# Optimization experiments

Measured on AMD Instinct MI355X. Metric: run time of the kernel, lower is better.

The kernel has to match this reference:

```python
import jax, jax.numpy as jnp
import numpy as np

B, M, D = 16384, 40, 32
INPUT_DIM = M * D  # 1280
CIN_SIZES = [128, 128]
DEEP_DIMS = [256, 128, 64]
EPS = 1e-5


def _init_linear(key, fan_in, fan_out):
    k1, k2 = jax.random.split(key)
    bound = 1.0 / np.sqrt(fan_in)
    w = jax.random.uniform(k1, (fan_out, fan_in), jnp.float32, -bound, bound)
    b = jax.random.uniform(k2, (fan_out,), jnp.float32, -bound, bound)
    return w, b


def setup_inputs() -> dict:
    key = jax.random.key(0)
    ks = jax.random.split(key, 12)
    x = jax.random.normal(ks[0], (B, INPUT_DIM), jnp.float32)
    emb_3d = jax.random.normal(ks[1], (B, M, D), jnp.float32)
    lin_w, lin_b = _init_linear(ks[2], INPUT_DIM, 1)
    # CIN conv1d (kernel_size=1) weights, flattened to [out, in]
    conv_w0, conv_b0 = _init_linear(ks[3], M * M, CIN_SIZES[0])          # in = 40*40
    prev1 = CIN_SIZES[0] // 2                                             # split_half
    conv_w1, conv_b1 = _init_linear(ks[4], M * prev1, CIN_SIZES[1])       # in = 40*64
    cin_out_dim = CIN_SIZES[0] // 2 + CIN_SIZES[1]                        # 192
    cin_out_w, cin_out_b = _init_linear(ks[5], cin_out_dim, 1)
    dims = [INPUT_DIM] + DEEP_DIMS
    deep_w0, deep_b0 = _init_linear(ks[6], dims[0], dims[1])
    deep_w1, deep_b1 = _init_linear(ks[7], dims[1], dims[2])
    deep_w2, deep_b2 = _init_linear(ks[8], dims[2], dims[3])
    ln_g0, ln_b0 = jnp.ones((dims[1],), jnp.float32), jnp.zeros((dims[1],), jnp.float32)
    ln_g1, ln_b1 = jnp.ones((dims[2],), jnp.float32), jnp.zeros((dims[2],), jnp.float32)
    ln_g2, ln_b2 = jnp.ones((dims[3],), jnp.float32), jnp.zeros((dims[3],), jnp.float32)
    return dict(x=x, emb_3d=emb_3d, lin_w=lin_w, lin_b=lin_b,
                conv_w0=conv_w0, conv_b0=conv_b0, conv_w1=conv_w1, conv_b1=conv_b1,
                cin_out_w=cin_out_w, cin_out_b=cin_out_b,
                deep_w0=deep_w0, deep_b0=deep_b0, ln_g0=ln_g0, ln_b0=ln_b0,
                deep_w1=deep_w1, deep_b1=deep_b1, ln_g1=ln_g1, ln_b1=ln_b1,
                deep_w2=deep_w2, deep_b2=deep_b2, ln_g2=ln_g2, ln_b2=ln_b2)


def _layernorm(h, g, b):
    mu = jnp.mean(h, axis=-1, keepdims=True)
    var = jnp.mean(jnp.square(h - mu), axis=-1, keepdims=True)
    return (h - mu) * jax.lax.rsqrt(var + EPS) * g + b


def _cin_layer(x0, xi, w, b):
    # outer = einsum('bmd,bnd->bmnd') then 1x1 conv over flattened (m*n).
    # Fused: contract the (m,n) outer product directly with the conv weight.
    o = w.shape[0]
    m, n = x0.shape[1], xi.shape[1]
    w3 = w.reshape(o, m, n)
    out = jnp.einsum('bmd,bnd,omn->bod', x0, xi, w3) + b[None, :, None]
    return jax.nn.relu(out)


def reference(x, emb_3d, lin_w, lin_b,
              conv_w0, conv_b0, conv_w1, conv_b1, cin_out_w, cin_out_b,
              deep_w0, deep_b0, ln_g0, ln_b0,
              deep_w1, deep_b1, ln_g1, ln_b1,
              deep_w2, deep_b2, ln_g2, ln_b2):
    aux = (x @ lin_w.T + lin_b)[:, 0]  # [B]

    # CIN with split_half=True
    x0 = emb_3d                                   # [B, 40, 32]
    out0 = _cin_layer(x0, x0, conv_w0, conv_b0)    # [B, 128, 32]
    h1, direct0 = jnp.split(out0, 2, axis=1)       # hidden gets FIRST half
    out1 = _cin_layer(x0, h1, conv_w1, conv_b1)    # [B, 128, 32]
    cin_feat = jnp.sum(jnp.concatenate([direct0, out1], axis=1), axis=2)  # [B, 192]
    aux = aux + (cin_feat @ cin_out_w.T + cin_out_b)[:, 0]

    # Deep tower (dropout = identity in eval)
    h = jax.nn.relu(_layernorm(x @ deep_w0.T + deep_b0, ln_g0, ln_b0))
    h = jax.nn.relu(_layernorm(h @ deep_w1.T + deep_b1, ln_g1, ln_b1))
    h = jax.nn.relu(_layernorm(h @ deep_w2.T + deep_b2, ln_g2, ln_b2))
    return h, aux
```

## Files before the change

kernel.cpp:

```cpp
#include <hip/hip_runtime.h>
#include <hip/hip_bf16.h>

typedef unsigned int u32;
typedef __attribute__((ext_vector_type(8))) short short8;
typedef __attribute__((ext_vector_type(8))) _Float16 half8;
typedef __attribute__((ext_vector_type(4))) float f32x4;

__device__ __forceinline__ u32 bf16_rne(float f) {
  u32 u = __builtin_bit_cast(u32, f);
  return (u + 0x7fffu + ((u >> 16) & 1u)) >> 16;
}
__device__ __forceinline__ u32 pk_bf16(float a, float b) {
  union { __hip_bfloat162 h; u32 u; } cv;
  cv.h = __float22bfloat162_rn(make_float2(a, b));
  return cv.u;
}
__device__ __forceinline__ unsigned short f16b(float f) {
  return __builtin_bit_cast(unsigned short, (_Float16)f);
}
__device__ __forceinline__ half8 splat8(_Float16 x) {
  return (half8){x, x, x, x, x, x, x, x};
}

__device__ __forceinline__ void glds16(const u32* g, u32* l) {
  __builtin_amdgcn_global_load_lds((const __attribute__((address_space(1))) u32*)g,
                                   (__attribute__((address_space(3))) u32*)l, 16, 0, 0);
}

__global__ void swz_kernel(const float* __restrict__ W, unsigned short* __restrict__ out,
                           int N, int K) {
  int tid = blockIdx.x * 256 + threadIdx.x;
  if (tid >= N * K) return;
  int j = tid & 7, l = (tid >> 3) & 63, rest = tid >> 9;
  int nt = N >> 4;
  int t = rest % nt, k32 = rest / nt;
  int o = t * 16 + (l & 15);
  int k = k32 * 32 + (l >> 4) * 8 + j;
  out[tid] = (unsigned short)bf16_rne(W[(size_t)o * K + k]);
}
__global__ void swz_f16_kernel(const float* __restrict__ W, unsigned short* __restrict__ out,
                               int N, int K) {
  int tid = blockIdx.x * 256 + threadIdx.x;
  if (tid >= N * K) return;
  int j = tid & 7, l = (tid >> 3) & 63, rest = tid >> 9;
  int nt = N >> 4;
  int t = rest % nt, k32 = rest / nt;
  int o = t * 16 + (l & 15);
  int k = k32 * 32 + (l >> 4) * 8 + j;
  out[tid] = f16b(W[(size_t)o * K + k]);
}

__global__ void tbl_kernel(u32* __restrict__ tbl0) {
  int g = threadIdx.x;
  if (g >= 120) return;
  int base = 0, m = 0;
  for (m = 0; m < 40; ++m) {
    int cnt = 5 - (m >> 3);
    if (g < base + cnt) break;
    base += cnt;
  }
  int n0 = 8 * ((m >> 3) + (g - base));
  tbl0[g] = (u32)m | ((u32)n0 << 8);
}

__global__ void swz0s_kernel(const float* __restrict__ W, const u32* __restrict__ tbl0,
                             unsigned short* __restrict__ out) {
  int tid = blockIdx.x * 256 + threadIdx.x;
  if (tid >= 960 * 128) return;
  int j = tid & 7, l = (tid >> 3) & 63, rest = tid >> 9;
  int t = rest & 7, k32 = rest >> 3;
  int o = t * 16 + (l & 15);
  int g = k32 * 4 + (l >> 4);
  u32 te = tbl0[g];
  int m = (int)(te & 255u), n0 = (int)(te >> 8);
  int n = n0 + j;
  float val;
  if (n < m) val = 0.f;
  else if (n == m) val = W[o * 1600 + m * 41];
  else val = W[o * 1600 + m * 40 + n] + W[o * 1600 + n * 40 + m];
  out[tid] = f16b(val);
}

__global__ void lin_kernel(const float* __restrict__ x, const float* __restrict__ lw,
                           const float* __restrict__ lb, const float* __restrict__ cb,
                           float* __restrict__ aux) {
  int row = blockIdx.x * 4 + (threadIdx.x >> 6);
  int lane = threadIdx.x & 63;
  const float* xr = x + (size_t)row * 1280;
  float s = 0.f;
#pragma unroll
  for (int e = 0; e < 20; ++e) s += xr[e * 64 + lane] * lw[e * 64 + lane];
#pragma unroll
  for (int m = 1; m < 64; m <<= 1) s += __shfl_xor(s, m, 64);
  if (lane == 0) aux[row] = s + lb[0] + cb[0];
}

__global__ __launch_bounds__(256, 4) void cin_kernel(
    const float* __restrict__ emb, const unsigned short* __restrict__ wz0s,
    const unsigned short* __restrict__ wz1, const u32* __restrict__ tbl0,
    const float* __restrict__ b0v, const float* __restrict__ b1v,
    const float* __restrict__ cw, float* __restrict__ aux) {
  __shared__ unsigned short Xh[128 * 44];
  __shared__ unsigned short h1s[128 * 68];
  __shared__ u32 tbl[120];
  __shared__ float auxacc[128];

  const int tid = threadIdx.x;
  const int lane = tid & 63;
  const int w = tid >> 6;
  const int wr = w >> 1, wc = w & 1;
  const int rl = lane & 15, q = lane >> 4;
  const int b0blk = blockIdx.x * 4;

#pragma unroll
  for (int i = 0; i < 5; ++i) {
    int idx = i * 256 + tid;
    int b = idx / 320;
    int rem = idx - b * 320;
    int m = rem >> 3, d0 = (rem & 7) * 4;
    float4 v = *(const float4*)(emb + ((size_t)(b0blk + b) * 40 + m) * 32 + d0);
    unsigned short* xc = &Xh[(b * 32 + d0) * 44 + m];
    xc[0] = f16b(v.x); xc[44] = f16b(v.y); xc[88] = f16b(v.z); xc[132] = f16b(v.w);
  }
  if (tid < 128) auxacc[tid] = 0.f;
  if (tid < 120) tbl[tid] = tbl0[tid];
  __syncthreads();

  f32x4 acc[4][4];
#pragma unroll
  for (int u = 0; u < 4; ++u)
#pragma unroll
    for (int t = 0; t < 4; ++t) acc[u][t] = f32x4{0.f, 0.f, 0.f, 0.f};

  {
    const u32* bptr = (const u32*)wz0s + wc * 1024 + lane * 4;
    uint4 bA[4], bB[4];
#pragma unroll
    for (int tt = 0; tt < 4; ++tt) bA[tt] = *(const uint4*)(bptr + tt * 256);

    auto chunk0 = [&](int kc, uint4* bv) {
      u32 te = tbl[kc * 4 + q];
      int mm = (int)(te & 255u);
      int w0 = (int)(te >> 8) >> 1;
#pragma unroll
      for (int u = 0; u < 4; ++u) {
        int r = 64 * wr + 16 * u + rl;
        const u32* xr = (const u32*)&Xh[r * 44];
        uint4 vn = *(const uint4*)&xr[w0];
        _Float16 xm = __builtin_bit_cast(_Float16, Xh[r * 44 + mm]);
        half8 af = __builtin_bit_cast(half8, vn) * splat8(xm);
#pragma unroll
        for (int tt = 0; tt < 4; ++tt)
          acc[u][tt] = __builtin_amdgcn_mfma_f32_16x16x32_f16(
              af, __builtin_bit_cast(half8, bv[tt]), acc[u][tt], 0, 0, 0);
      }
    };

    for (int kc = 0; kc < 30; kc += 2) {
#pragma unroll
      for (int tt = 0; tt < 4; ++tt)
        bB[tt] = *(const uint4*)(bptr + (kc + 1) * 2048 + tt * 256);
      chunk0(kc, bA);
      int kn2 = (kc + 2 < 30) ? kc + 2 : 0;
#pragma unroll
      for (int tt = 0; tt < 4; ++tt)
        bA[tt] = *(const uint4*)(bptr + kn2 * 2048 + tt * 256);
      chunk0(kc + 1, bB);
    }
  }

  if (wc == 0) {
#pragma unroll
    for (int u = 0; u < 4; ++u) {
      int r0q = 64 * wr + 16 * u + 4 * q;
#pragma unroll
      for (int tt = 0; tt < 4; ++tt) {
        int o = 16 * tt + rl;
        float bb = b0v[o];
#pragma unroll
        for (int i = 0; i < 4; ++i) {
          float vv = fmaxf(acc[u][tt][i] + bb, 0.f);
          h1s[(r0q + i) * 68 + o] = f16b(vv);
        }
      }
    }
  } else {
#pragma unroll
    for (int u = 0; u < 4; ++u)
#pragma unroll
      for (int i = 0; i < 4; ++i) {
        float sle = 0.f;
#pragma unroll
        for (int tt = 0; tt < 4; ++tt) {
          int o = 64 + 16 * tt + rl;
          sle += fmaxf(acc[u][tt][i] + b0v[o], 0.f) * cw[o - 64];
        }
        sle += __shfl_xor(sle, 1, 16);
        sle += __shfl_xor(sle, 2, 16);
        sle += __shfl_xor(sle, 4, 16);
        sle += __shfl_xor(sle, 8, 16);
        if (rl == 0) atomicAdd(&auxacc[64 * wr + 16 * u + 4 * q + i], sle);
      }
  }
#pragma unroll
  for (int u = 0; u < 4; ++u)
#pragma unroll
    for (int t = 0; t < 4; ++t) acc[u][t] = f32x4{0.f, 0.f, 0.f, 0.f};
  __syncthreads();

  {
    const u32* bptr = (const u32*)wz1 + wc * 1024 + lane * 4;
    uint4 bA[4], bB[4];
#pragma unroll
    for (int tt = 0; tt < 4; ++tt) bA[tt] = *(const uint4*)(bptr + tt * 256);

    auto chunk1 = [&](int kc, uint4* bv) {
      int mm = kc >> 1;
      int wof = ((kc & 1) << 4) + 4 * q;
#pragma unroll
      for (int u = 0; u < 4; ++u) {
        int r = 64 * wr + 16 * u + rl;
        uint4 hp = *(const uint4*)((const u32*)h1s + r * 34 + wof);
        _Float16 xm = __builtin_bit_cast(_Float16, Xh[r * 44 + mm]);
        half8 af = __builtin_bit_cast(half8, hp) * splat8(xm);
#pragma unroll
        for (int tt = 0; tt < 4; ++tt)
          acc[u][tt] = __builtin_amdgcn_mfma_f32_16x16x32_f16(
              af, __builtin_bit_cast(half8, bv[tt]), acc[u][tt], 0, 0, 0);
      }
    };

    for (int kc = 0; kc < 80; kc += 2) {
#pragma unroll
      for (int tt = 0; tt < 4; ++tt)
        bB[tt] = *(const uint4*)(bptr + (kc + 1) * 2048 + tt * 256);
      chunk1(kc, bA);
      int kn2 = (kc + 2 < 80) ? kc + 2 : 0;
#pragma unroll
      for (int tt = 0; tt < 4; ++tt)
        bA[tt] = *(const uint4*)(bptr + kn2 * 2048 + tt * 256);
      chunk1(kc + 1, bB);
    }
  }

#pragma unroll
  for (int u = 0; u < 4; ++u)
#pragma unroll
    for (int i = 0; i < 4; ++i) {
      float sle = 0.f;
#pragma unroll
      for (int tt = 0; tt < 4; ++tt) {
        int o = 64 * wc + 16 * tt + rl;
        sle += fmaxf(acc[u][tt][i] + b1v[o], 0.f) * cw[64 + o];
      }
      sle += __shfl_xor(sle, 1, 16);
      sle += __shfl_xor(sle, 2, 16);
      sle += __shfl_xor(sle, 4, 16);
      sle += __shfl_xor(sle, 8, 16);
      if (rl == 0) atomicAdd(&auxacc[64 * wr + 16 * u + 4 * q + i], sle);
    }
  __syncthreads();
  if (tid < 4) {
    float ssum = 0.f;
    for (int d = 0; d < 32; ++d) ssum += auxacc[tid * 32 + d];
    aux[b0blk + tid] += ssum;
  }
}

template <int NT, bool AF32>
__global__ __launch_bounds__(256, 2) void gemm_deep(
    const void* __restrict__ Ain, const unsigned short* __restrict__ Bswz,
    const float* __restrict__ bias, float* __restrict__ Cout, int M, int N, int K) {
  __shared__ unsigned short At[128 * 40];
  __shared__ u32 Bt[NT * 256];
  const int tid = threadIdx.x, lane = tid & 63, w = tid >> 6;
  const int wr = w >> 1, wc = w & 1, rl = lane & 15, q = lane >> 4;
  const int r0 = blockIdx.x * 128, c0 = blockIdx.y * (NT * 16);
  const int ntg = N >> 4;
  constexpr int WT = NT / 2;
  f32x4 acc[4][WT];
#pragma unroll
  for (int u = 0; u < 4; ++u)
#pragma unroll
    for (int t = 0; t < WT; ++t) acc[u][t] = f32x4{0.f, 0.f, 0.f, 0.f};

  for (int kk = 0; kk < K; kk += 32) {
    __syncthreads();
    {
      int r = tid >> 1, kh = (tid & 1) * 16;
      if constexpr (AF32) {
        const float* A = (const float*)Ain;
        const float* src = A + (size_t)(r0 + r) * K + kk + kh;
        float4 v0 = *(const float4*)src;
        float4 v1 = *(const float4*)(src + 4);
        float4 v2 = *(const float4*)(src + 8);
        float4 v3 = *(const float4*)(src + 12);
        uint4 p0, p1;
        p0.x = pk_bf16(v0.x, v0.y); p0.y = pk_bf16(v0.z, v0.w);
        p0.z = pk_bf16(v1.x, v1.y); p0.w = pk_bf16(v1.z, v1.w);
        p1.x = pk_bf16(v2.x, v2.y); p1.y = pk_bf16(v2.z, v2.w);
        p1.z = pk_bf16(v3.x, v3.y); p1.w = pk_bf16(v3.z, v3.w);
        uint4* dst = (uint4*)&At[r * 40 + kh];
        dst[0] = p0;
        dst[1] = p1;
      } else {
        const unsigned short* A = (const unsigned short*)Ain;
        const uint4* src = (const uint4*)(A + (size_t)(r0 + r) * K + kk + kh);
        uint4* dst = (uint4*)&At[r * 40 + kh];
        dst[0] = src[0];
        dst[1] = src[1];
      }
      const u32* gb = (const u32*)Bswz + ((size_t)(kk >> 5) * ntg + (c0 >> 4)) * 256;
      constexpr int WW = NT * 64;
#pragma unroll
      for (int j = 0; j < NT / 4; ++j)
        glds16(gb + w * WW + j * 256 + lane * 4, &Bt[w * WW + j * 256]);
    }
    __syncthreads();
    short8 af[4];
#pragma unroll
    for (int u = 0; u < 4; ++u) {
      int rt = 4 * wr + u;
      uint4 av = *(const uint4*)&At[(16 * rt + rl) * 40 + q * 8];
      af[u] = __builtin_bit_cast(short8, av);
    }
#pragma unroll
    for (int tt = 0; tt < WT; ++tt) {
      int tg = WT * wc + tt;
      uint4 bv = *(const uint4*)&Bt[(tg * 64 + lane) * 4];
      short8 bfv = __builtin_bit_cast(short8, bv);
#pragma unroll
      for (int u = 0; u < 4; ++u)
        acc[u][tt] = __builtin_amdgcn_mfma_f32_16x16x32_bf16(af[u], bfv, acc[u][tt], 0, 0, 0);
    }
  }
#pragma unroll
  for (int u = 0; u < 4; ++u) {
    int rr = r0 + 64 * wr + 16 * u + 4 * q;
#pragma unroll
    for (int tt = 0; tt < WT; ++tt) {
      int o = c0 + (WT * wc + tt) * 16 + rl;
      float bb = bias[o];
#pragma unroll
      for (int i = 0; i < 4; ++i)
        Cout[(size_t)(rr + i) * N + o] = acc[u][tt][i] + bb;
    }
  }
}

template <int D, bool OUTF32>
__global__ void ln_relu_kernel(const float* __restrict__ in, const float* __restrict__ g,
                               const float* __restrict__ bt, void* __restrict__ out) {
  int row = blockIdx.x * 4 + (threadIdx.x >> 6);
  int lane = threadIdx.x & 63;
  constexpr int E = D / 64;
  const float* src = in + (size_t)row * D;
  float v[E], s1 = 0.f, s2 = 0.f;
#pragma unroll
  for (int e = 0; e < E; ++e) {
    v[e] = src[e * 64 + lane];
    s1 += v[e];
    s2 += v[e] * v[e];
  }
#pragma unroll
  for (int m = 1; m < 64; m <<= 1) {
    s1 += __shfl_xor(s1, m, 64);
    s2 += __shfl_xor(s2, m, 64);
  }
  float mu = s1 / (float)D;
  float rs = rsqrtf(s2 / (float)D - mu * mu + 1e-5f);
#pragma unroll
  for (int e = 0; e < E; ++e) {
    int c = e * 64 + lane;
    float y = fmaxf((v[e] - mu) * rs * g[c] + bt[c], 0.f);
    if constexpr (OUTF32)
      ((float*)out)[(size_t)row * D + c] = y;
    else
      ((unsigned short*)out)[(size_t)row * D + c] = (unsigned short)bf16_rne(y);
  }
}

extern "C" void kernel_launch(void* const* d_in, const int* in_sizes, int n_in,
                              void* d_out, int out_size, void* d_ws, size_t ws_size,
                              hipStream_t stream) {
  const float* x = (const float*)d_in[0];
  const float* emb = (const float*)d_in[1];
  const float* lin_w = (const float*)d_in[2];
  const float* lin_b = (const float*)d_in[3];
  const float* cw0 = (const float*)d_in[4];
  const float* cb0 = (const float*)d_in[5];
  const float* cw1 = (const float*)d_in[6];
  const float* cb1 = (const float*)d_in[7];
  const float* cow = (const float*)d_in[8];
  const float* cob = (const float*)d_in[9];
  const float* dw0 = (const float*)d_in[10];
  const float* db0 = (const float*)d_in[11];
  const float* g0 = (const float*)d_in[12];
  const float* be0 = (const float*)d_in[13];
  const float* dw1 = (const float*)d_in[14];
  const float* db1 = (const float*)d_in[15];
  const float* g1 = (const float*)d_in[16];
  const float* be1 = (const float*)d_in[17];
  const float* dw2 = (const float*)d_in[18];
  const float* db2 = (const float*)d_in[19];
  const float* g2 = (const float*)d_in[20];
  const float* be2 = (const float*)d_in[21];

  char* ws = (char*)d_ws;
  unsigned short* wz0s = (unsigned short*)(ws + 0);
  u32* tbl0 = (u32*)(ws + 245760);
  unsigned short* wz1 = (unsigned short*)(ws + 246272);
  unsigned short* wzd0 = (unsigned short*)(ws + 901632);
  unsigned short* wzd1 = (unsigned short*)(ws + 1556992);
  unsigned short* wzd2 = (unsigned short*)(ws + 1622528);
  float* t0 = (float*)(ws + 1638912);
  unsigned short* h0b = (unsigned short*)(ws + 18416128);
  float* t1 = (float*)(ws + 26804736);
  unsigned short* h1b = (unsigned short*)(ws + 35193344);
  float* t2 = (float*)(ws + 39387648);

  float* h_out = (float*)d_out;
  float* aux = h_out + (size_t)16384 * 64;

  tbl_kernel<<<1, 128, 0, stream>>>(tbl0);
  swz0s_kernel<<<480, 256, 0, stream>>>(cw0, tbl0, wz0s);
  swz_f16_kernel<<<(2560 * 128 + 255) / 256, 256, 0, stream>>>(cw1, wz1, 128, 2560);
  swz_kernel<<<(1280 * 256 + 255) / 256, 256, 0, stream>>>(dw0, wzd0, 256, 1280);
  swz_kernel<<<(256 * 128 + 255) / 256, 256, 0, stream>>>(dw1, wzd1, 128, 256);
  swz_kernel<<<(128 * 64 + 255) / 256, 256, 0, stream>>>(dw2, wzd2, 64, 128);

  lin_kernel<<<4096, 256, 0, stream>>>(x, lin_w, lin_b, cob, aux);
  cin_kernel<<<4096, 256, 0, stream>>>(emb, wz0s, wz1, tbl0, cb0, cb1, cow, aux);

  gemm_deep<8, true><<<dim3(128, 2), 256, 0, stream>>>(x, wzd0, db0, t0, 16384, 256, 1280);
  ln_relu_kernel<256, false><<<4096, 256, 0, stream>>>(t0, g0, be0, h0b);
  gemm_deep<8, false><<<dim3(128, 1), 256, 0, stream>>>(h0b, wzd1, db1, t1, 16384, 128, 256);
  ln_relu_kernel<128, false><<<4096, 256, 0, stream>>>(t1, g1, be1, h1b);
  gemm_deep<4, false><<<dim3(128, 1), 256, 0, stream>>>(h1b, wzd2, db2, t2, 16384, 64, 128);
  ln_relu_kernel<64, true><<<4096, 256, 0, stream>>>(t2, g2, be2, h_out);
}
```

Before: 721.0 us.

## Give each CIN wave all 128 rows with 128-thread blocks and MFMA priority

The CIN kernel moves from four waves (2x2 row/column split) to two waves per block. Each wave now covers all 128 rows with 8x4 MFMA accumulator tiles, so every B-fragment load is reused across twice as many MFMAs. The layer-1 loop hoists the per-row x0 scale loads so both K-halves share them, and s_setprio is raised around the MFMA bursts. The linear kernel switches to float4 loads. The cost is doubled accumulator registers with launch bounds of (128,2), which may cut occupancy and latency hiding.

```diff
diff --git a/kernel.cpp b/kernel.cpp
--- a/kernel.cpp
+++ b/kernel.cpp
@@ -86,16 +86,21 @@
                            float* __restrict__ aux) {
   int row = blockIdx.x * 4 + (threadIdx.x >> 6);
   int lane = threadIdx.x & 63;
-  const float* xr = x + (size_t)row * 1280;
+  const float4* xr = (const float4*)(x + (size_t)row * 1280);
+  const float4* lw4 = (const float4*)lw;
   float s = 0.f;
 #pragma unroll
-  for (int e = 0; e < 20; ++e) s += xr[e * 64 + lane] * lw[e * 64 + lane];
+  for (int e = 0; e < 5; ++e) {
+    float4 a = xr[e * 64 + lane];
+    float4 b = lw4[e * 64 + lane];
+    s += a.x * b.x + a.y * b.y + a.z * b.z + a.w * b.w;
+  }
 #pragma unroll
   for (int m = 1; m < 64; m <<= 1) s += __shfl_xor(s, m, 64);
   if (lane == 0) aux[row] = s + lb[0] + cb[0];
 }
 
-__global__ __launch_bounds__(256, 4) void cin_kernel(
+__global__ __launch_bounds__(128, 2) void cin_kernel(
     const float* __restrict__ emb, const unsigned short* __restrict__ wz0s,
     const unsigned short* __restrict__ wz1, const u32* __restrict__ tbl0,
     const float* __restrict__ b0v, const float* __restrict__ b1v,
@@ -107,14 +112,13 @@
 
   const int tid = threadIdx.x;
   const int lane = tid & 63;
-  const int w = tid >> 6;
-  const int wr = w >> 1, wc = w & 1;
+  const int wc = tid >> 6;
   const int rl = lane & 15, q = lane >> 4;
   const int b0blk = blockIdx.x * 4;
 
 #pragma unroll
-  for (int i = 0; i < 5; ++i) {
-    int idx = i * 256 + tid;
+  for (int i = 0; i < 10; ++i) {
+    int idx = i * 128 + tid;
     int b = idx / 320;
     int rem = idx - b * 320;
     int m = rem >> 3, d0 = (rem & 7) * 4;
@@ -122,13 +126,13 @@
     unsigned short* xc = &Xh[(b * 32 + d0) * 44 + m];
     xc[0] = f16b(v.x); xc[44] = f16b(v.y); xc[88] = f16b(v.z); xc[132] = f16b(v.w);
   }
-  if (tid < 128) auxacc[tid] = 0.f;
+  auxacc[tid] = 0.f;
   if (tid < 120) tbl[tid] = tbl0[tid];
   __syncthreads();
 
-  f32x4 acc[4][4];
-#pragma unroll
-  for (int u = 0; u < 4; ++u)
+  f32x4 acc[8][4];
+#pragma unroll
+  for (int u = 0; u < 8; ++u)
 #pragma unroll
     for (int t = 0; t < 4; ++t) acc[u][t] = f32x4{0.f, 0.f, 0.f, 0.f};
 
@@ -143,16 +147,18 @@
       int mm = (int)(te & 255u);
       int w0 = (int)(te >> 8) >> 1;
 #pragma unroll
-      for (int u = 0; u < 4; ++u) {
-        int r = 64 * wr + 16 * u + rl;
+      for (int u = 0; u < 8; ++u) {
+        int r = 16 * u + rl;
         const u32* xr = (const u32*)&Xh[r * 44];
         uint4 vn = *(const uint4*)&xr[w0];
         _Float16 xm = __builtin_bit_cast(_Float16, Xh[r * 44 + mm]);
         half8 af = __builtin_bit_cast(half8, vn) * splat8(xm);
+        __builtin_amdgcn_s_setprio(1);
 #pragma unroll
         for (int tt = 0; tt < 4; ++tt)
           acc[u][tt] = __builtin_amdgcn_mfma_f32_16x16x32_f16(
               af, __builtin_bit_cast(half8, bv[tt]), acc[u][tt], 0, 0, 0);
+        __builtin_amdgcn_s_setprio(0);
       }
     };
 
@@ -171,8 +177,8 @@
 
   if (wc == 0) {
 #pragma unroll
-    for (int u = 0; u < 4; ++u) {
-      int r0q = 64 * wr + 16 * u + 4 * q;
+    for (int u = 0; u < 8; ++u) {
+      int r0q = 16 * u + 4 * q;
 #pragma unroll
       for (int tt = 0; tt < 4; ++tt) {
         int o = 16 * tt + rl;
@@ -186,7 +192,7 @@
     }
   } else {
 #pragma unroll
-    for (int u = 0; u < 4; ++u)
+    for (int u = 0; u < 8; ++u)
 #pragma unroll
       for (int i = 0; i < 4; ++i) {
         float sle = 0.f;
@@ -199,11 +205,11 @@
         sle += __shfl_xor(sle, 2, 16);
         sle += __shfl_xor(sle, 4, 16);
         sle += __shfl_xor(sle, 8, 16);
-        if (rl == 0) atomicAdd(&auxacc[64 * wr + 16 * u + 4 * q + i], sle);
-      }
-  }
-#pragma unroll
-  for (int u = 0; u < 4; ++u)
+        if (rl == 0) atomicAdd(&auxacc[16 * u + 4 * q + i], sle);
+      }
+  }
+#pragma unroll
+  for (int u = 0; u < 8; ++u)
 #pragma unroll
     for (int t = 0; t < 4; ++t) acc[u][t] = f32x4{0.f, 0.f, 0.f, 0.f};
   __syncthreads();
@@ -214,37 +220,41 @@
 #pragma unroll
     for (int tt = 0; tt < 4; ++tt) bA[tt] = *(const uint4*)(bptr + tt * 256);
 
-    auto chunk1 = [&](int kc, uint4* bv) {
-      int mm = kc >> 1;
-      int wof = ((kc & 1) << 4) + 4 * q;
-#pragma unroll
-      for (int u = 0; u < 4; ++u) {
-        int r = 64 * wr + 16 * u + rl;
+    auto chunk1 = [&](int wof, uint4* bv, const _Float16* xmv) {
+#pragma unroll
+      for (int u = 0; u < 8; ++u) {
+        int r = 16 * u + rl;
         uint4 hp = *(const uint4*)((const u32*)h1s + r * 34 + wof);
-        _Float16 xm = __builtin_bit_cast(_Float16, Xh[r * 44 + mm]);
-        half8 af = __builtin_bit_cast(half8, hp) * splat8(xm);
+        half8 af = __builtin_bit_cast(half8, hp) * splat8(xmv[u]);
+        __builtin_amdgcn_s_setprio(1);
 #pragma unroll
         for (int tt = 0; tt < 4; ++tt)
           acc[u][tt] = __builtin_amdgcn_mfma_f32_16x16x32_f16(
               af, __builtin_bit_cast(half8, bv[tt]), acc[u][tt], 0, 0, 0);
+        __builtin_amdgcn_s_setprio(0);
       }
     };
 
-    for (int kc = 0; kc < 80; kc += 2) {
+    for (int kp = 0; kp < 40; ++kp) {
+      int kc = 2 * kp;
 #pragma unroll
       for (int tt = 0; tt < 4; ++tt)
         bB[tt] = *(const uint4*)(bptr + (kc + 1) * 2048 + tt * 256);
-      chunk1(kc, bA);
+      _Float16 xmv[8];
+#pragma unroll
+      for (int u = 0; u < 8; ++u)
+        xmv[u] = __builtin_bit_cast(_Float16, Xh[(16 * u + rl) * 44 + kp]);
+      chunk1(4 * q, bA, xmv);
       int kn2 = (kc + 2 < 80) ? kc + 2 : 0;
 #pragma unroll
       for (int tt = 0; tt < 4; ++tt)
         bA[tt] = *(const uint4*)(bptr + kn2 * 2048 + tt * 256);
-      chunk1(kc + 1, bB);
-    }
-  }
-
-#pragma unroll
-  for (int u = 0; u < 4; ++u)
+      chunk1(16 + 4 * q, bB, xmv);
+    }
+  }
+
+#pragma unroll
+  for (int u = 0; u < 8; ++u)
 #pragma unroll
     for (int i = 0; i < 4; ++i) {
       float sle = 0.f;
@@ -257,7 +267,7 @@
       sle += __shfl_xor(sle, 2, 16);
       sle += __shfl_xor(sle, 4, 16);
       sle += __shfl_xor(sle, 8, 16);
-      if (rl == 0) atomicAdd(&auxacc[64 * wr + 16 * u + 4 * q + i], sle);
+      if (rl == 0) atomicAdd(&auxacc[16 * u + 4 * q + i], sle);
     }
   __syncthreads();
   if (tid < 4) {
@@ -430,7 +440,7 @@
   swz_kernel<<<(128 * 64 + 255) / 256, 256, 0, stream>>>(dw2, wzd2, 64, 128);
 
   lin_kernel<<<4096, 256, 0, stream>>>(x, lin_w, lin_b, cob, aux);
-  cin_kernel<<<4096, 256, 0, stream>>>(emb, wz0s, wz1, tbl0, cb0, cb1, cow, aux);
+  cin_kernel<<<4096, 128, 0, stream>>>(emb, wz0s, wz1, tbl0, cb0, cb1, cow, aux);
 
   gemm_deep<8, true><<<dim3(128, 2), 256, 0, stream>>>(x, wzd0, db0, t0, 16384, 256, 1280);
   ln_relu_kernel<256, false><<<4096, 256, 0, stream>>>(t0, g0, be0, h0b);
```

Result: slower. 748.8 us (+3.9%).

## Software-pipeline LDS operand loads in CIN MFMA loops and vectorize linear kernel

Applied to the files above, without the earlier changes.

The CIN kernel's two MFMA loops now prefetch the next chunk's LDS operands (X rows, h1 rows, scale values) into registers alongside the global weight loads, and raise wave priority around the MFMA bursts. LDS row strides change (44 to 40, 68 to 72) with 16-byte alignment, and launch bounds drop from 4 to 2 waves per SIMD to leave room for the extra registers. The linear aux kernel switches to float4 loads. The goal is to hide LDS latency behind matrix work, at the cost of lower occupancy and possible LDS bank conflicts with the new strides.

```diff
diff --git a/kernel.cpp b/kernel.cpp
--- a/kernel.cpp
+++ b/kernel.cpp
@@ -86,22 +86,27 @@
                            float* __restrict__ aux) {
   int row = blockIdx.x * 4 + (threadIdx.x >> 6);
   int lane = threadIdx.x & 63;
-  const float* xr = x + (size_t)row * 1280;
+  const float4* xr = (const float4*)(x + (size_t)row * 1280);
+  const float4* lw4 = (const float4*)lw;
   float s = 0.f;
 #pragma unroll
-  for (int e = 0; e < 20; ++e) s += xr[e * 64 + lane] * lw[e * 64 + lane];
+  for (int e = 0; e < 5; ++e) {
+    float4 a = xr[e * 64 + lane];
+    float4 b = lw4[e * 64 + lane];
+    s += a.x * b.x + a.y * b.y + a.z * b.z + a.w * b.w;
+  }
 #pragma unroll
   for (int m = 1; m < 64; m <<= 1) s += __shfl_xor(s, m, 64);
   if (lane == 0) aux[row] = s + lb[0] + cb[0];
 }
 
-__global__ __launch_bounds__(256, 4) void cin_kernel(
+__global__ __launch_bounds__(256, 2) void cin_kernel(
     const float* __restrict__ emb, const unsigned short* __restrict__ wz0s,
     const unsigned short* __restrict__ wz1, const u32* __restrict__ tbl0,
     const float* __restrict__ b0v, const float* __restrict__ b1v,
     const float* __restrict__ cw, float* __restrict__ aux) {
-  __shared__ unsigned short Xh[128 * 44];
-  __shared__ unsigned short h1s[128 * 68];
+  __shared__ __align__(16) unsigned short Xh[128 * 40];
+  __shared__ __align__(16) unsigned short h1s[128 * 72];
   __shared__ u32 tbl[120];
   __shared__ float auxacc[128];
 
@@ -119,8 +124,8 @@
     int rem = idx - b * 320;
     int m = rem >> 3, d0 = (rem & 7) * 4;
     float4 v = *(const float4*)(emb + ((size_t)(b0blk + b) * 40 + m) * 32 + d0);
-    unsigned short* xc = &Xh[(b * 32 + d0) * 44 + m];
-    xc[0] = f16b(v.x); xc[44] = f16b(v.y); xc[88] = f16b(v.z); xc[132] = f16b(v.w);
+    unsigned short* xc = &Xh[(b * 32 + d0) * 40 + m];
+    xc[0] = f16b(v.x); xc[40] = f16b(v.y); xc[80] = f16b(v.z); xc[120] = f16b(v.w);
   }
   if (tid < 128) auxacc[tid] = 0.f;
   if (tid < 120) tbl[tid] = tbl0[tid];
@@ -134,38 +139,49 @@
 
   {
     const u32* bptr = (const u32*)wz0s + wc * 1024 + lane * 4;
+    const u32* xw = (const u32*)Xh;
     uint4 bA[4], bB[4];
-#pragma unroll
-    for (int tt = 0; tt < 4; ++tt) bA[tt] = *(const uint4*)(bptr + tt * 256);
-
-    auto chunk0 = [&](int kc, uint4* bv) {
+    uint4 vnA[4], vnB[4];
+    _Float16 xmA[4], xmB[4];
+
+    auto loadB0 = [&](int kc, uint4* b) {
+#pragma unroll
+      for (int tt = 0; tt < 4; ++tt) b[tt] = *(const uint4*)(bptr + kc * 2048 + tt * 256);
+    };
+    auto loadA0 = [&](int kc, uint4* vn, _Float16* xm) {
       u32 te = tbl[kc * 4 + q];
       int mm = (int)(te & 255u);
       int w0 = (int)(te >> 8) >> 1;
 #pragma unroll
       for (int u = 0; u < 4; ++u) {
         int r = 64 * wr + 16 * u + rl;
-        const u32* xr = (const u32*)&Xh[r * 44];
-        uint4 vn = *(const uint4*)&xr[w0];
-        _Float16 xm = __builtin_bit_cast(_Float16, Xh[r * 44 + mm]);
-        half8 af = __builtin_bit_cast(half8, vn) * splat8(xm);
+        vn[u] = *(const uint4*)(xw + r * 20 + w0);
+        xm[u] = __builtin_bit_cast(_Float16, Xh[r * 40 + mm]);
+      }
+    };
+    auto mfma0 = [&](const uint4* vn, const _Float16* xm, const uint4* bv) {
+      __builtin_amdgcn_s_setprio(1);
+#pragma unroll
+      for (int u = 0; u < 4; ++u) {
+        half8 af = __builtin_bit_cast(half8, vn[u]) * splat8(xm[u]);
 #pragma unroll
         for (int tt = 0; tt < 4; ++tt)
           acc[u][tt] = __builtin_amdgcn_mfma_f32_16x16x32_f16(
               af, __builtin_bit_cast(half8, bv[tt]), acc[u][tt], 0, 0, 0);
       }
-    };
-
+      __builtin_amdgcn_s_setprio(0);
+    };
+
+    loadB0(0, bA);
+    loadA0(0, vnA, xmA);
     for (int kc = 0; kc < 30; kc += 2) {
-#pragma unroll
-      for (int tt = 0; tt < 4; ++tt)
-        bB[tt] = *(const uint4*)(bptr + (kc + 1) * 2048 + tt * 256);
-      chunk0(kc, bA);
-      int kn2 = (kc + 2 < 30) ? kc + 2 : 0;
-#pragma unroll
-      for (int tt = 0; tt < 4; ++tt)
-        bA[tt] = *(const uint4*)(bptr + kn2 * 2048 + tt * 256);
-      chunk0(kc + 1, bB);
+      loadB0(kc + 1, bB);
+      loadA0(kc + 1, vnB, xmB);
+      mfma0(vnA, xmA, bA);
+      int kn = (kc + 2 < 30) ? kc + 2 : 0;
+      loadB0(kn, bA);
+      loadA0(kn, vnA, xmA);
+      mfma0(vnB, xmB, bB);
     }
   }
 
@@ -180,7 +196,7 @@
 #pragma unroll
         for (int i = 0; i < 4; ++i) {
           float vv = fmaxf(acc[u][tt][i] + bb, 0.f);
-          h1s[(r0q + i) * 68 + o] = f16b(vv);
+          h1s[(r0q + i) * 72 + o] = f16b(vv);
         }
       }
     }
@@ -210,36 +226,57 @@
 
   {
     const u32* bptr = (const u32*)wz1 + wc * 1024 + lane * 4;
+    const u32* hw = (const u32*)h1s;
     uint4 bA[4], bB[4];
-#pragma unroll
-    for (int tt = 0; tt < 4; ++tt) bA[tt] = *(const uint4*)(bptr + tt * 256);
-
-    auto chunk1 = [&](int kc, uint4* bv) {
-      int mm = kc >> 1;
+    uint4 hpA[4], hpB[4];
+    _Float16 xmA[4], xmB[4];
+
+    auto loadB1 = [&](int kc, uint4* b) {
+#pragma unroll
+      for (int tt = 0; tt < 4; ++tt) b[tt] = *(const uint4*)(bptr + kc * 2048 + tt * 256);
+    };
+    auto loadH = [&](int kc, uint4* hp) {
       int wof = ((kc & 1) << 4) + 4 * q;
 #pragma unroll
       for (int u = 0; u < 4; ++u) {
         int r = 64 * wr + 16 * u + rl;
-        uint4 hp = *(const uint4*)((const u32*)h1s + r * 34 + wof);
-        _Float16 xm = __builtin_bit_cast(_Float16, Xh[r * 44 + mm]);
-        half8 af = __builtin_bit_cast(half8, hp) * splat8(xm);
+        hp[u] = *(const uint4*)(hw + r * 36 + wof);
+      }
+    };
+    auto loadXM = [&](int kp, _Float16* xm) {
+#pragma unroll
+      for (int u = 0; u < 4; ++u)
+        xm[u] = __builtin_bit_cast(_Float16, Xh[(64 * wr + 16 * u + rl) * 40 + kp]);
+    };
+    auto mfma1 = [&](const uint4* hp, const _Float16* xm, const uint4* bv) {
+      __builtin_amdgcn_s_setprio(1);
+#pragma unroll
+      for (int u = 0; u < 4; ++u) {
+        half8 af = __builtin_bit_cast(half8, hp[u]) * splat8(xm[u]);
 #pragma unroll
         for (int tt = 0; tt < 4; ++tt)
           acc[u][tt] = __builtin_amdgcn_mfma_f32_16x16x32_f16(
               af, __builtin_bit_cast(half8, bv[tt]), acc[u][tt], 0, 0, 0);
       }
-    };
-
-    for (int kc = 0; kc < 80; kc += 2) {
-#pragma unroll
-      for (int tt = 0; tt < 4; ++tt)
-        bB[tt] = *(const uint4*)(bptr + (kc + 1) * 2048 + tt * 256);
-      chunk1(kc, bA);
-      int kn2 = (kc + 2 < 80) ? kc + 2 : 0;
-#pragma unroll
-      for (int tt = 0; tt < 4; ++tt)
-        bA[tt] = *(const uint4*)(bptr + kn2 * 2048 + tt * 256);
-      chunk1(kc + 1, bB);
+      __builtin_amdgcn_s_setprio(0);
+    };
+
+    loadB1(0, bA);
+    loadH(0, hpA);
+    loadXM(0, xmA);
+    for (int kp = 0; kp < 40; ++kp) {
+      int kc = 2 * kp;
+      loadB1(kc + 1, bB);
+      loadH(kc + 1, hpB);
+      mfma1(hpA, xmA, bA);
+      int kc2 = (kc + 2 < 80) ? kc + 2 : 0;
+      int kn = (kp + 1 < 40) ? kp + 1 : 0;
+      loadB1(kc2, bA);
+      loadH(kc2, hpA);
+      loadXM(kn, xmB);
+      mfma1(hpB, xmA, bB);
+#pragma unroll
+      for (int u = 0; u < 4; ++u) xmA[u] = xmB[u];
     }
   }
 
```

Measured after the change: 627.1 us. -13.0%, faster.
